# Kernel tuning notes

Hardware: AMD Instinct MI355X
Metric: run time of the kernel (lower is better)

The kernel has to match this reference:

```python
import jax, jax.numpy as jnp
import numpy as np

N_NODES = 100000
N_EDGES = 600000
D = 128          # embedding_dim == hidden_dim
OUT = 128        # output_dim
L = 5            # number of GINConv layers


def setup_inputs() -> dict:
    key = jax.random.key(0)
    ks = jax.random.split(key, 9)
    return {
        "x": jax.random.randint(ks[0], (N_NODES,), 0, N_NODES),
        "edge_index": jax.random.randint(ks[1], (2, N_EDGES), 0, N_NODES),
        "emb": jax.random.normal(ks[2], (N_NODES, D), dtype=jnp.float32) * 0.02,
        "Wa": jax.random.normal(ks[3], (L, D, D), dtype=jnp.float32) * 0.05,
        "ba": jnp.zeros((L, D), dtype=jnp.float32),
        "Wb": jax.random.normal(ks[4], (L, D, D), dtype=jnp.float32) * 0.05,
        "bb": jnp.zeros((L, D), dtype=jnp.float32),
        "Wlin": jax.random.normal(ks[5], (D, OUT), dtype=jnp.float32) * 0.05,
        "blin": jnp.zeros((OUT,), dtype=jnp.float32),
    }


def reference(x, edge_index, emb, Wa, ba, Wb, bb, Wlin, blin):
    src, dst = edge_index[0], edge_index[1]
    h = emb[x]  # [N, D] embedding lookup
    for l in range(L):
        # GINConv with eps=0: mlp((1+eps)*x_i + sum_{j->i} x_j)
        agg = jax.ops.segment_sum(h[src], dst, num_segments=N_NODES)  # [N, D]
        z = h + agg
        z = jax.nn.relu(z @ Wa[l] + ba[l])  # MLP hidden
        z = z @ Wb[l] + bb[l]               # MLP out
        h = jax.nn.relu(z)                  # outer F.relu in forward
    pooled = jnp.sum(h, axis=0, keepdims=True)  # global_add_pool, batch=None -> [1, D]
    return pooled @ Wlin + blin                  # [1, OUT]
```

## Files before the change

kernel.cpp:

```cpp
#include <hip/hip_runtime.h>

#define D 128
#define NLAYERS 5

using short8  = __attribute__((ext_vector_type(8))) short;
using short4v = __attribute__((ext_vector_type(4))) short;
using floatx4 = __attribute__((ext_vector_type(4))) float;
using floatx2 = __attribute__((ext_vector_type(2))) float;

__device__ __forceinline__ unsigned bf16_rne(float x) {
    unsigned u = __float_as_uint(x);
    return (u + 0x7fffu + ((u >> 16) & 1u)) >> 16;
}
__device__ __forceinline__ float bf16_to_f32(short s) {
    return __uint_as_float(((unsigned)(unsigned short)s) << 16);
}

#define HSCALE 16.0f
#define HSCALE_INV 0.0625f

__global__ void prepA_kernel(const int* __restrict__ x, const float* __restrict__ emb,
                             const float* __restrict__ Wa, const float* __restrict__ Wb,
                             const int* __restrict__ edst,
                             unsigned char* __restrict__ H0, short* __restrict__ wt,
                             int* __restrict__ deg,
                             int n_nodes, int n_edges) {
    const int gtid = blockIdx.x * 256 + threadIdx.x;
    const int gsz  = gridDim.x * 256;
    for (int g = gtid; g < 2 * NLAYERS * D * D; g += gsz) {
        int mat = g >> 14, idx = g & 16383;
        int n = idx >> 7, k = idx & 127;
        const float* W = (mat & 1) ? (Wb + (size_t)(mat >> 1) * D * D)
                                   : (Wa + (size_t)(mat >> 1) * D * D);
        wt[g] = (short)bf16_rne(W[k * D + n]);
    }
    for (int t = gtid; t < n_nodes * 32; t += gsz) {
        int node = t >> 5, lane = t & 31;
        int s = x[node];
        const float4 v = *reinterpret_cast<const float4*>(emb + (size_t)s * D + lane * 4);
        int w = __builtin_amdgcn_cvt_pk_fp8_f32(v.x * HSCALE, v.y * HSCALE, 0, false);
        w = __builtin_amdgcn_cvt_pk_fp8_f32(v.z * HSCALE, v.w * HSCALE, w, true);
        reinterpret_cast<unsigned int*>(H0)[(size_t)node * 32 + lane] = (unsigned int)w;
    }
    for (int e = gtid; e < n_edges; e += gsz) atomicAdd(&deg[edst[e]], 1);
}

#define SCAN_TILE 1024
__global__ void scan_sums_kernel(const int* __restrict__ deg, int* __restrict__ bsums, int n) {
    __shared__ int red[256];
    int base = blockIdx.x * SCAN_TILE + threadIdx.x * 4;
    int s = 0;
    #pragma unroll
    for (int j = 0; j < 4; j++) {
        int i = base + j;
        if (i < n) s += deg[i];
    }
    red[threadIdx.x] = s;
    __syncthreads();
    for (int off = 128; off > 0; off >>= 1) {
        if (threadIdx.x < off) red[threadIdx.x] += red[threadIdx.x + off];
        __syncthreads();
    }
    if (threadIdx.x == 0) bsums[blockIdx.x] = red[0];
}

__global__ void scan_bsums_kernel(int* __restrict__ bsums, int nblocks) {
    __shared__ int sdata[256];
    int carry = 0;
    for (int base = 0; base < nblocks; base += 256) {
        int i = base + threadIdx.x;
        int v = (i < nblocks) ? bsums[i] : 0;
        sdata[threadIdx.x] = v;
        __syncthreads();
        for (int off = 1; off < 256; off <<= 1) {
            int t = (threadIdx.x >= off) ? sdata[threadIdx.x - off] : 0;
            __syncthreads();
            sdata[threadIdx.x] += t;
            __syncthreads();
        }
        int incl = sdata[threadIdx.x];
        if (i < nblocks) bsums[i] = carry + incl - v;
        carry += sdata[255];
        __syncthreads();
    }
}

__global__ void scan_final_kernel(const int* __restrict__ deg, const int* __restrict__ bsums,
                                  int* __restrict__ offsets, int* __restrict__ cursor, int n) {
    __shared__ int sdata[256];
    int base = blockIdx.x * SCAN_TILE + threadIdx.x * 4;
    int v[4];
    int s = 0;
    #pragma unroll
    for (int j = 0; j < 4; j++) {
        int i = base + j;
        v[j] = (i < n) ? deg[i] : 0;
        s += v[j];
    }
    sdata[threadIdx.x] = s;
    __syncthreads();
    for (int off = 1; off < 256; off <<= 1) {
        int t = (threadIdx.x >= off) ? sdata[threadIdx.x - off] : 0;
        __syncthreads();
        sdata[threadIdx.x] += t;
        __syncthreads();
    }
    int excl = sdata[threadIdx.x] - s + bsums[blockIdx.x];
    #pragma unroll
    for (int j = 0; j < 4; j++) {
        int i = base + j;
        if (i <= n) offsets[i] = excl;
        if (i < n) cursor[i] = excl;
        excl += v[j];
    }
}

__global__ void fill_kernel(const int* __restrict__ esrc, const int* __restrict__ edst,
                            int* __restrict__ cursor, int* __restrict__ csr_src, int n_edges) {
    int e = blockIdx.x * 256 + threadIdx.x;
    if (e >= n_edges) return;
    int pos = atomicAdd(&cursor[edst[e]], 1);
    csr_src[pos] = esrc[e];
}

__global__ __launch_bounds__(256) void agg_kernel(
        const int* __restrict__ offsets, const int* __restrict__ csr_src,
        const unsigned char* __restrict__ h_in, short* __restrict__ z, int n_rows) {
    const int t   = blockIdx.x * 256 + threadIdx.x;
    const int row = t >> 3;
    const int l8  = t & 7;
    if (row >= n_rows) return;

    float acc[16];
    {
        uint4 w = *reinterpret_cast<const uint4*>(h_in + (size_t)row * D + l8 * 16);
        unsigned int wd[4] = {w.x, w.y, w.z, w.w};
        #pragma unroll
        for (int k = 0; k < 4; k++) {
            floatx2 lo = __builtin_amdgcn_cvt_pk_f32_fp8((int)wd[k], false);
            floatx2 hi = __builtin_amdgcn_cvt_pk_f32_fp8((int)wd[k], true);
            acc[4 * k]     = lo[0]; acc[4 * k + 1] = lo[1];
            acc[4 * k + 2] = hi[0]; acc[4 * k + 3] = hi[1];
        }
    }
    int e   = offsets[row];
    int end = offsets[row + 1];
    for (; e + 3 < end; e += 4) {
        int sA = csr_src[e];
        int sB = csr_src[e + 1];
        int sC = csr_src[e + 2];
        int sD = csr_src[e + 3];
        uint4 wA = *reinterpret_cast<const uint4*>(h_in + (size_t)sA * D + l8 * 16);
        uint4 wB = *reinterpret_cast<const uint4*>(h_in + (size_t)sB * D + l8 * 16);
        uint4 wC = *reinterpret_cast<const uint4*>(h_in + (size_t)sC * D + l8 * 16);
        uint4 wD = *reinterpret_cast<const uint4*>(h_in + (size_t)sD * D + l8 * 16);
        unsigned int da[4] = {wA.x, wA.y, wA.z, wA.w};
        unsigned int db[4] = {wB.x, wB.y, wB.z, wB.w};
        unsigned int dc[4] = {wC.x, wC.y, wC.z, wC.w};
        unsigned int dd[4] = {wD.x, wD.y, wD.z, wD.w};
        #pragma unroll
        for (int k = 0; k < 4; k++) {
            floatx2 alo = __builtin_amdgcn_cvt_pk_f32_fp8((int)da[k], false);
            floatx2 ahi = __builtin_amdgcn_cvt_pk_f32_fp8((int)da[k], true);
            floatx2 blo = __builtin_amdgcn_cvt_pk_f32_fp8((int)db[k], false);
            floatx2 bhi = __builtin_amdgcn_cvt_pk_f32_fp8((int)db[k], true);
            floatx2 clo = __builtin_amdgcn_cvt_pk_f32_fp8((int)dc[k], false);
            floatx2 chi = __builtin_amdgcn_cvt_pk_f32_fp8((int)dc[k], true);
            floatx2 dlo = __builtin_amdgcn_cvt_pk_f32_fp8((int)dd[k], false);
            floatx2 dhi = __builtin_amdgcn_cvt_pk_f32_fp8((int)dd[k], true);
            acc[4 * k]     += (alo[0] + blo[0]) + (clo[0] + dlo[0]);
            acc[4 * k + 1] += (alo[1] + blo[1]) + (clo[1] + dlo[1]);
            acc[4 * k + 2] += (ahi[0] + bhi[0]) + (chi[0] + dhi[0]);
            acc[4 * k + 3] += (ahi[1] + bhi[1]) + (chi[1] + dhi[1]);
        }
    }
    for (; e < end; e++) {
        int sA = csr_src[e];
        uint4 wA = *reinterpret_cast<const uint4*>(h_in + (size_t)sA * D + l8 * 16);
        unsigned int da[4] = {wA.x, wA.y, wA.z, wA.w};
        #pragma unroll
        for (int k = 0; k < 4; k++) {
            floatx2 alo = __builtin_amdgcn_cvt_pk_f32_fp8((int)da[k], false);
            floatx2 ahi = __builtin_amdgcn_cvt_pk_f32_fp8((int)da[k], true);
            acc[4 * k]     += alo[0];
            acc[4 * k + 1] += alo[1];
            acc[4 * k + 2] += ahi[0];
            acc[4 * k + 3] += ahi[1];
        }
    }
    short8 o0, o1;
    #pragma unroll
    for (int j = 0; j < 8; j++) {
        o0[j] = (short)bf16_rne(acc[j] * HSCALE_INV);
        o1[j] = (short)bf16_rne(acc[8 + j] * HSCALE_INV);
    }
    const int c0 = 2 * l8, c1 = 2 * l8 + 1;
    *reinterpret_cast<short8*>(z + ((size_t)row * 16 + (c0 ^ (row & 15))) * 8) = o0;
    *reinterpret_cast<short8*>(z + ((size_t)row * 16 + (c1 ^ (row & 15))) * 8) = o1;
}

__global__ __launch_bounds__(512, 6) void mlp_kernel(
        const short* __restrict__ z, const short* __restrict__ wta,
        const short* __restrict__ wtb, const float* __restrict__ ba,
        const float* __restrict__ bb, unsigned char* __restrict__ h_out,
        float* __restrict__ pooled_accum, int n_rows) {
    __shared__ __align__(16) short zsh[64 * 128];
    __shared__ __align__(16) short wsh[128 * 128];

    const int tid  = threadIdx.x;
    const int row0 = blockIdx.x * 64;

    #pragma unroll
    for (int i = 0; i < 4; i++) {
        int g = i * 512 + tid;
        int n = g >> 4, c = g & 15;
        int off = (n * 16 + (c ^ (n & 15))) * 8;
        *reinterpret_cast<short8*>(&wsh[off]) =
            *reinterpret_cast<const short8*>(wta + n * D + c * 8);
    }
    #pragma unroll
    for (int i = 0; i < 2; i++) {
        int idx = i * 512 + tid;
        int r = idx >> 4;
        short8 v;
        if (row0 + r < n_rows)
            v = *reinterpret_cast<const short8*>(z + ((size_t)row0 * 16 + idx) * 8);
        else
            v = short8{0, 0, 0, 0, 0, 0, 0, 0};
        *reinterpret_cast<short8*>(&zsh[idx * 8]) = v;
    }
    __syncthreads();

    const int lane = tid & 63;
    const int wave = tid >> 6;
    const int wr   = wave >> 1;
    const int wc   = wave & 1;
    const int lm   = lane & 15;
    const int quad = lane >> 4;

    floatx4 acc1[4];
    #pragma unroll
    for (int b = 0; b < 4; b++) acc1[b] = floatx4{0.f, 0.f, 0.f, 0.f};
    {
        const int r = wr * 16 + lm;
        #pragma unroll
        for (int ks = 0; ks < 4; ks++) {
            const int c = ks * 4 + quad;
            short8 av = *reinterpret_cast<const short8*>(&zsh[(r * 16 + (c ^ (r & 15))) * 8]);
            #pragma unroll
            for (int cs = 0; cs < 4; cs++) {
                int nn = wc * 64 + cs * 16 + lm;
                short8 bv = *reinterpret_cast<const short8*>(&wsh[(nn * 16 + (c ^ (nn & 15))) * 8]);
                acc1[cs] = __builtin_amdgcn_mfma_f32_16x16x32_bf16(av, bv, acc1[cs], 0, 0, 0);
            }
        }
    }
    __syncthreads();

    #pragma unroll
    for (int i = 0; i < 4; i++) {
        int g = i * 512 + tid;
        int n = g >> 4, c = g & 15;
        int off = (n * 16 + (c ^ (n & 15))) * 8;
        *reinterpret_cast<short8*>(&wsh[off]) =
            *reinterpret_cast<const short8*>(wtb + n * D + c * 8);
    }

    #pragma unroll
    for (int cs = 0; cs < 4; cs++) {
        int col = wc * 64 + cs * 16 + lm;
        float bva = ba[col];
        int cj = col >> 3, ci = col & 7;
        #pragma unroll
        for (int reg = 0; reg < 4; reg++) {
            int r = wr * 16 + quad * 4 + reg;
            float v = fmaxf(acc1[cs][reg] + bva, 0.f);
            zsh[(r * 16 + (cj ^ (r & 15))) * 8 + ci] = (short)bf16_rne(v);
        }
    }
    __syncthreads();

    floatx4 acc2[4];
    #pragma unroll
    for (int b = 0; b < 4; b++) acc2[b] = floatx4{0.f, 0.f, 0.f, 0.f};
    {
        const int r = wr * 16 + lm;
        #pragma unroll
        for (int ks = 0; ks < 4; ks++) {
            const int c = ks * 4 + quad;
            short8 av = *reinterpret_cast<const short8*>(&zsh[(r * 16 + (c ^ (r & 15))) * 8]);
            #pragma unroll
            for (int cs = 0; cs < 4; cs++) {
                int nn = wc * 64 + cs * 16 + lm;
                short8 bv = *reinterpret_cast<const short8*>(&wsh[(nn * 16 + (c ^ (nn & 15))) * 8]);
                acc2[cs] = __builtin_amdgcn_mfma_f32_16x16x32_bf16(av, bv, acc2[cs], 0, 0, 0);
            }
        }
    }

    float psum[4];
    #pragma unroll
    for (int cs = 0; cs < 4; cs++) {
        int col = wc * 64 + cs * 16 + lm;
        float bvb = bb[col];
        float s = 0.f;
        #pragma unroll
        for (int reg = 0; reg < 4; reg++) {
            int r = row0 + wr * 16 + quad * 4 + reg;
            if (r < n_rows) {
                float v = fmaxf(acc2[cs][reg] + bvb, 0.f);
                if (h_out != nullptr) {
                    float sv = v * HSCALE;
                    int pw = __builtin_amdgcn_cvt_pk_fp8_f32(sv, sv, 0, false);
                    h_out[(size_t)r * D + col] = (unsigned char)(pw & 0xff);
                }
                s += v;
            }
        }
        psum[cs] = s;
    }

    if (pooled_accum != nullptr) {
        __syncthreads();
        float* part = (float*)zsh;
        #pragma unroll
        for (int cs = 0; cs < 4; cs++)
            part[(wr * 4 + quad) * 128 + wc * 64 + cs * 16 + lm] = psum[cs];
        __syncthreads();
        if (tid < 128) {
            float s = 0.f;
            #pragma unroll
            for (int g = 0; g < 16; g++) s += part[g * 128 + tid];
            atomicAdd(&pooled_accum[tid], s);
        }
    }
}

__global__ void final_kernel(const float* __restrict__ pooled, const float* __restrict__ Wlin,
                             const float* __restrict__ blin, float* __restrict__ out) {
    const int j = threadIdx.x;
    __shared__ float p[D];
    p[j] = pooled[j];
    __syncthreads();
    float s = blin[j];
    #pragma unroll 8
    for (int k = 0; k < D; k++) s += p[k] * Wlin[k * D + j];
    out[j] = s;
}

extern "C" void kernel_launch(void* const* d_in, const int* in_sizes, int n_in,
                              void* d_out, int out_size, void* d_ws, size_t ws_size,
                              hipStream_t stream) {
    const int*   x    = (const int*)d_in[0];
    const int*   ei   = (const int*)d_in[1];
    const float* emb  = (const float*)d_in[2];
    const float* Wa   = (const float*)d_in[3];
    const float* ba   = (const float*)d_in[4];
    const float* Wb   = (const float*)d_in[5];
    const float* bb   = (const float*)d_in[6];
    const float* Wlin = (const float*)d_in[7];
    const float* blin = (const float*)d_in[8];
    float* out = (float*)d_out;

    const int N = in_sizes[0];
    const int E = in_sizes[1] / 2;
    const int* esrc = ei;
    const int* edst = ei + E;

    unsigned char* H0 = (unsigned char*)d_ws;
    unsigned char* H1 = H0 + (size_t)N * D;
    short* zbuf = (short*)(H1 + (size_t)N * D);
    float* pooled = (float*)(zbuf + (size_t)N * D);
    int* deg     = (int*)(pooled + 128);
    int* offsets = deg + N;
    int* cursor  = offsets + (N + 1);
    int* bsums   = cursor + N;
    int* csr_src = bsums + 4096;
    uintptr_t wt_addr = ((uintptr_t)(csr_src + E) + 15) & ~(uintptr_t)15;
    short* wt = (short*)wt_addr;

    const int scan_blocks = (N + 1 + SCAN_TILE - 1) / SCAN_TILE;

    hipMemsetAsync(pooled, 0, (size_t)(128 + N) * sizeof(int), stream);

    prepA_kernel<<<1024, 256, 0, stream>>>(x, emb, Wa, Wb, edst, H0, wt, deg, N, E);
    scan_sums_kernel<<<scan_blocks, 256, 0, stream>>>(deg, bsums, N);
    scan_bsums_kernel<<<1, 256, 0, stream>>>(bsums, scan_blocks);
    scan_final_kernel<<<scan_blocks, 256, 0, stream>>>(deg, bsums, offsets, cursor, N);
    fill_kernel<<<(E + 255) / 256, 256, 0, stream>>>(esrc, edst, cursor, csr_src, E);

    const int agg_blocks = (N * 8 + 255) / 256;
    const int mlp_blocks = (N + 63) / 64;
    unsigned char* hin = H0; unsigned char* hout = H1;
    for (int l = 0; l < NLAYERS; l++) {
        const bool last = (l == NLAYERS - 1);
        float* pacc = last ? pooled : nullptr;
        unsigned char* hdst = last ? nullptr : hout;
        agg_kernel<<<agg_blocks, 256, 0, stream>>>(offsets, csr_src, hin, zbuf, N);
        mlp_kernel<<<mlp_blocks, 512, 0, stream>>>(
            zbuf, wt + (size_t)(2 * l) * D * D, wt + (size_t)(2 * l + 1) * D * D,
            ba + (size_t)l * D, bb + (size_t)l * D, hdst, pacc, N);
        unsigned char* tmp = hin; hin = hout; hout = tmp;
    }

    final_kernel<<<1, 128, 0, stream>>>(pooled, Wlin, blin, out);
}
```

Measured before the change: 415.4 us.

## Make MLP kernel persistent with per-wave 16-row tiles and resident weights

Result: no change. 415.1 us (-0.1%).

```diff
diff --git a/kernel.cpp b/kernel.cpp
--- a/kernel.cpp
+++ b/kernel.cpp
@@ -194,144 +194,139 @@
         o0[j] = (short)bf16_rne(acc[j] * HSCALE_INV);
         o1[j] = (short)bf16_rne(acc[8 + j] * HSCALE_INV);
     }
-    const int c0 = 2 * l8, c1 = 2 * l8 + 1;
-    *reinterpret_cast<short8*>(z + ((size_t)row * 16 + (c0 ^ (row & 15))) * 8) = o0;
-    *reinterpret_cast<short8*>(z + ((size_t)row * 16 + (c1 ^ (row & 15))) * 8) = o1;
-}
-
-__global__ __launch_bounds__(512, 6) void mlp_kernel(
+    *reinterpret_cast<short8*>(z + (size_t)row * D + l8 * 16)     = o0;
+    *reinterpret_cast<short8*>(z + (size_t)row * D + l8 * 16 + 8) = o1;
+}
+
+__global__ __launch_bounds__(256, 2) void mlp_kernel(
         const short* __restrict__ z, const short* __restrict__ wta,
         const short* __restrict__ wtb, const float* __restrict__ ba,
         const float* __restrict__ bb, unsigned char* __restrict__ h_out,
-        float* __restrict__ pooled_accum, int n_rows) {
-    __shared__ __align__(16) short zsh[64 * 128];
-    __shared__ __align__(16) short wsh[128 * 128];
-
-    const int tid  = threadIdx.x;
-    const int row0 = blockIdx.x * 64;
-
-    #pragma unroll
-    for (int i = 0; i < 4; i++) {
-        int g = i * 512 + tid;
+        float* __restrict__ pooled_accum, int n_rows, int n_tiles) {
+    __shared__ __align__(16) short wash[128 * 128];
+    __shared__ __align__(16) short wbsh[128 * 128];
+    __shared__ __align__(16) short tsh[4][16 * 128];
+
+    const int tid = threadIdx.x;
+
+    #pragma unroll
+    for (int i = 0; i < 8; i++) {
+        int g = i * 256 + tid;
         int n = g >> 4, c = g & 15;
         int off = (n * 16 + (c ^ (n & 15))) * 8;
-        *reinterpret_cast<short8*>(&wsh[off]) =
+        *reinterpret_cast<short8*>(&wash[off]) =
             *reinterpret_cast<const short8*>(wta + n * D + c * 8);
-    }
-    #pragma unroll
-    for (int i = 0; i < 2; i++) {
-        int idx = i * 512 + tid;
-        int r = idx >> 4;
-        short8 v;
-        if (row0 + r < n_rows)
-            v = *reinterpret_cast<const short8*>(z + ((size_t)row0 * 16 + idx) * 8);
-        else
-            v = short8{0, 0, 0, 0, 0, 0, 0, 0};
-        *reinterpret_cast<short8*>(&zsh[idx * 8]) = v;
+        *reinterpret_cast<short8*>(&wbsh[off]) =
+            *reinterpret_cast<const short8*>(wtb + n * D + c * 8);
     }
     __syncthreads();
 
     const int lane = tid & 63;
-    const int wave = tid >> 6;
-    const int wr   = wave >> 1;
-    const int wc   = wave & 1;
+    const int wv   = tid >> 6;
     const int lm   = lane & 15;
     const int quad = lane >> 4;
-
-    floatx4 acc1[4];
-    #pragma unroll
-    for (int b = 0; b < 4; b++) acc1[b] = floatx4{0.f, 0.f, 0.f, 0.f};
-    {
-        const int r = wr * 16 + lm;
+    short* myt = &tsh[wv][0];
+
+    float bva[8], bvb[8];
+    #pragma unroll
+    for (int cs = 0; cs < 8; cs++) {
+        bva[cs] = ba[cs * 16 + lm];
+        bvb[cs] = bb[cs * 16 + lm];
+    }
+
+    float poolsum[8];
+    #pragma unroll
+    for (int cs = 0; cs < 8; cs++) poolsum[cs] = 0.f;
+
+    const int wave_id = blockIdx.x * 4 + wv;
+    const int n_waves = gridDim.x * 4;
+
+    for (int tile = wave_id; tile < n_tiles; tile += n_waves) {
+        const int row0 = tile * 16;
+        const int r    = row0 + lm;
+
+        short8 av[4];
+        #pragma unroll
+        for (int ks = 0; ks < 4; ks++) {
+            if (r < n_rows)
+                av[ks] = *reinterpret_cast<const short8*>(z + (size_t)r * D + (ks * 4 + quad) * 8);
+            else
+                av[ks] = short8{0, 0, 0, 0, 0, 0, 0, 0};
+        }
+
+        floatx4 acc1[8];
+        #pragma unroll
+        for (int cs = 0; cs < 8; cs++) acc1[cs] = floatx4{0.f, 0.f, 0.f, 0.f};
         #pragma unroll
         for (int ks = 0; ks < 4; ks++) {
             const int c = ks * 4 + quad;
-            short8 av = *reinterpret_cast<const short8*>(&zsh[(r * 16 + (c ^ (r & 15))) * 8]);
             #pragma unroll
-            for (int cs = 0; cs < 4; cs++) {
-                int nn = wc * 64 + cs * 16 + lm;
-                short8 bv = *reinterpret_cast<const short8*>(&wsh[(nn * 16 + (c ^ (nn & 15))) * 8]);
-                acc1[cs] = __builtin_amdgcn_mfma_f32_16x16x32_bf16(av, bv, acc1[cs], 0, 0, 0);
+            for (int cs = 0; cs < 8; cs++) {
+                int nn = cs * 16 + lm;
+                short8 bv = *reinterpret_cast<const short8*>(&wash[(nn * 16 + (c ^ (nn & 15))) * 8]);
+                acc1[cs] = __builtin_amdgcn_mfma_f32_16x16x32_bf16(av[ks], bv, acc1[cs], 0, 0, 0);
             }
         }
-    }
-    __syncthreads();
-
-    #pragma unroll
-    for (int i = 0; i < 4; i++) {
-        int g = i * 512 + tid;
-        int n = g >> 4, c = g & 15;
-        int off = (n * 16 + (c ^ (n & 15))) * 8;
-        *reinterpret_cast<short8*>(&wsh[off]) =
-            *reinterpret_cast<const short8*>(wtb + n * D + c * 8);
-    }
-
-    #pragma unroll
-    for (int cs = 0; cs < 4; cs++) {
-        int col = wc * 64 + cs * 16 + lm;
-        float bva = ba[col];
-        int cj = col >> 3, ci = col & 7;
-        #pragma unroll
-        for (int reg = 0; reg < 4; reg++) {
-            int r = wr * 16 + quad * 4 + reg;
-            float v = fmaxf(acc1[cs][reg] + bva, 0.f);
-            zsh[(r * 16 + (cj ^ (r & 15))) * 8 + ci] = (short)bf16_rne(v);
-        }
-    }
-    __syncthreads();
-
-    floatx4 acc2[4];
-    #pragma unroll
-    for (int b = 0; b < 4; b++) acc2[b] = floatx4{0.f, 0.f, 0.f, 0.f};
-    {
-        const int r = wr * 16 + lm;
+
+        #pragma unroll
+        for (int cs = 0; cs < 8; cs++) {
+            int col = cs * 16 + lm;
+            int cj = col >> 3, ci = col & 7;
+            #pragma unroll
+            for (int reg = 0; reg < 4; reg++) {
+                int tr = quad * 4 + reg;
+                float v = fmaxf(acc1[cs][reg] + bva[cs], 0.f);
+                myt[(tr * 16 + (cj ^ tr)) * 8 + ci] = (short)bf16_rne(v);
+            }
+        }
+
+        short8 av2[4];
         #pragma unroll
         for (int ks = 0; ks < 4; ks++) {
             const int c = ks * 4 + quad;
-            short8 av = *reinterpret_cast<const short8*>(&zsh[(r * 16 + (c ^ (r & 15))) * 8]);
+            av2[ks] = *reinterpret_cast<const short8*>(&myt[(lm * 16 + (c ^ lm)) * 8]);
+        }
+
+        floatx4 acc2[8];
+        #pragma unroll
+        for (int cs = 0; cs < 8; cs++) acc2[cs] = floatx4{0.f, 0.f, 0.f, 0.f};
+        #pragma unroll
+        for (int ks = 0; ks < 4; ks++) {
+            const int c = ks * 4 + quad;
             #pragma unroll
-            for (int cs = 0; cs < 4; cs++) {
-                int nn = wc * 64 + cs * 16 + lm;
-                short8 bv = *reinterpret_cast<const short8*>(&wsh[(nn * 16 + (c ^ (nn & 15))) * 8]);
-                acc2[cs] = __builtin_amdgcn_mfma_f32_16x16x32_bf16(av, bv, acc2[cs], 0, 0, 0);
+            for (int cs = 0; cs < 8; cs++) {
+                int nn = cs * 16 + lm;
+                short8 bv = *reinterpret_cast<const short8*>(&wbsh[(nn * 16 + (c ^ (nn & 15))) * 8]);
+                acc2[cs] = __builtin_amdgcn_mfma_f32_16x16x32_bf16(av2[ks], bv, acc2[cs], 0, 0, 0);
             }
         }
-    }
-
-    float psum[4];
-    #pragma unroll
-    for (int cs = 0; cs < 4; cs++) {
-        int col = wc * 64 + cs * 16 + lm;
-        float bvb = bb[col];
-        float s = 0.f;
-        #pragma unroll
-        for (int reg = 0; reg < 4; reg++) {
-            int r = row0 + wr * 16 + quad * 4 + reg;
-            if (r < n_rows) {
-                float v = fmaxf(acc2[cs][reg] + bvb, 0.f);
-                if (h_out != nullptr) {
-                    float sv = v * HSCALE;
-                    int pw = __builtin_amdgcn_cvt_pk_fp8_f32(sv, sv, 0, false);
-                    h_out[(size_t)r * D + col] = (unsigned char)(pw & 0xff);
+
+        #pragma unroll
+        for (int cs = 0; cs < 8; cs++) {
+            int col = cs * 16 + lm;
+            #pragma unroll
+            for (int reg = 0; reg < 4; reg++) {
+                int rr = row0 + quad * 4 + reg;
+                if (rr < n_rows) {
+                    float v = fmaxf(acc2[cs][reg] + bvb[cs], 0.f);
+                    if (h_out != nullptr) {
+                        float sv = v * HSCALE;
+                        int pw = __builtin_amdgcn_cvt_pk_fp8_f32(sv, sv, 0, false);
+                        h_out[(size_t)rr * D + col] = (unsigned char)(pw & 0xff);
+                    }
+                    poolsum[cs] += v;
                 }
-                s += v;
             }
         }
-        psum[cs] = s;
     }
 
     if (pooled_accum != nullptr) {
-        __syncthreads();
-        float* part = (float*)zsh;
-        #pragma unroll
-        for (int cs = 0; cs < 4; cs++)
-            part[(wr * 4 + quad) * 128 + wc * 64 + cs * 16 + lm] = psum[cs];
-        __syncthreads();
-        if (tid < 128) {
-            float s = 0.f;
-            #pragma unroll
-            for (int g = 0; g < 16; g++) s += part[g * 128 + tid];
-            atomicAdd(&pooled_accum[tid], s);
+        #pragma unroll
+        for (int cs = 0; cs < 8; cs++) {
+            float v = poolsum[cs];
+            v += __shfl_xor(v, 16);
+            v += __shfl_xor(v, 32);
+            if (quad == 0) atomicAdd(&pooled_accum[cs * 16 + lm], v);
         }
     }
 }
@@ -390,16 +385,16 @@
     fill_kernel<<<(E + 255) / 256, 256, 0, stream>>>(esrc, edst, cursor, csr_src, E);
 
     const int agg_blocks = (N * 8 + 255) / 256;
-    const int mlp_blocks = (N + 63) / 64;
+    const int n_tiles    = (N + 15) / 16;
     unsigned char* hin = H0; unsigned char* hout = H1;
     for (int l = 0; l < NLAYERS; l++) {
         const bool last = (l == NLAYERS - 1);
         float* pacc = last ? pooled : nullptr;
         unsigned char* hdst = last ? nullptr : hout;
         agg_kernel<<<agg_blocks, 256, 0, stream>>>(offsets, csr_src, hin, zbuf, N);
-        mlp_kernel<<<mlp_blocks, 512, 0, stream>>>(
+        mlp_kernel<<<512, 256, 0, stream>>>(
             zbuf, wt + (size_t)(2 * l) * D * D, wt + (size_t)(2 * l + 1) * D * D,
-            ba + (size_t)l * D, bb + (size_t)l * D, hdst, pacc, N);
+            ba + (size_t)l * D, bb + (size_t)l * D, hdst, pacc, N, n_tiles);
         unsigned char* tmp = hin; hin = hout; hout = tmp;
     }
 
```
